# Kernel optimization log

Measured on AMD Instinct MI355X. Metric: run time of the kernel, lower is better.

## Reference

```python
import jax, jax.numpy as jnp
import numpy as np

N_NODES = 100000
N_EDGES = 1600000
N_FEAT = 128
HIDDEN = 64
N_CLASSES = 40


def setup_inputs() -> dict:
    key = jax.random.key(0)
    ks = jax.random.split(key, 4)
    x = jax.random.normal(ks[0], (N_NODES, N_FEAT), dtype=jnp.float32)
    edge_index = jax.random.randint(ks[1], (2, N_EDGES), 0, N_NODES, dtype=jnp.int64)
    # Glorot-style init like PyG GCNConv
    W1 = jax.random.normal(ks[2], (N_FEAT, HIDDEN), dtype=jnp.float32) * (1.0 / np.sqrt(N_FEAT))
    b1 = jnp.zeros((HIDDEN,), dtype=jnp.float32)
    W2 = jax.random.normal(ks[3], (HIDDEN, N_CLASSES), dtype=jnp.float32) * (1.0 / np.sqrt(HIDDEN))
    b2 = jnp.zeros((N_CLASSES,), dtype=jnp.float32)
    return {"x": x, "edge_index": edge_index, "W1": W1, "b1": b1, "W2": W2, "b2": b2}


def _gcn_conv(x, src, dst, norm, W, b, n_nodes):
    # PyG GCNConv: transform first, then normalized scatter-add aggregation
    h = x @ W                                   # [N, out]
    msg = h[src] * norm[:, None]                # [E+N, out] gather
    out = jax.ops.segment_sum(msg, dst, num_segments=n_nodes)  # scatter-add
    return out + b


def _norm_and_loops(edge_index, n_nodes):
    # add self-loops, symmetric normalization deg^{-1/2} A_hat deg^{-1/2}
    loop = jnp.arange(n_nodes, dtype=edge_index.dtype)
    src = jnp.concatenate([edge_index[0], loop])
    dst = jnp.concatenate([edge_index[1], loop])
    deg = jax.ops.segment_sum(jnp.ones_like(dst, dtype=jnp.float32), dst, num_segments=n_nodes)
    dinv = jnp.where(deg > 0, jax.lax.rsqrt(jnp.maximum(deg, 1.0)), 0.0)
    norm = dinv[src] * dinv[dst]
    return src, dst, norm


def reference(x, edge_index, W1, b1, W2, b2):
    n_nodes = x.shape[0]
    src, dst, norm = _norm_and_loops(edge_index, n_nodes)
    h = _gcn_conv(x, src, dst, norm, W1, b1, n_nodes)
    h = jax.nn.relu(h)
    h = _gcn_conv(h, src, dst, norm, W2, b2, n_nodes)
    return jax.nn.log_softmax(h, axis=1)
```

## Files before the change

### kernel.cpp

```cpp
#include <hip/hip_runtime.h>
#include <hip/hip_bf16.h>
#include <string.h>

#define N_FEAT 128
#define HIDDEN 64
#define N_CLS  40
#define SCAN_B 256
#define FILL_BLOCKS 1024
#define CHUNK_EDGES 2048

typedef __bf16 bf16x8 __attribute__((ext_vector_type(8)));
typedef float  f32x4  __attribute__((ext_vector_type(4)));

union Frag { unsigned u[4]; bf16x8 v; };

static __device__ inline int get_xcc() {
    return (int)(__builtin_amdgcn_s_getreg((3 << 11) | 20) & 7u);
}


static __device__ inline unsigned pack_bf16(float a, float b) {
    unsigned ba = __float_as_uint(a);
    unsigned bb = __float_as_uint(b);
    unsigned ra = (ba + 0x7fffu + ((ba >> 16) & 1u)) >> 16;
    unsigned rb = (bb + 0x7fffu + ((bb >> 16) & 1u)) >> 16;
    return (ra & 0xffffu) | (rb << 16);
}

static __device__ inline float2 unpack_bf16(unsigned v) {
    return make_float2(__uint_as_float(v << 16), __uint_as_float(v & 0xffff0000u));
}


__global__ void detect_layout_kernel(const int* __restrict__ ei, int* __restrict__ flag) {
    int lane = threadIdx.x;
    int v = ei[2 * lane + 1];
    unsigned long long b = __ballot(v != 0);
    if (lane == 0) flag[0] = (b == 0ull) ? 1 : 0;
}


__global__ __launch_bounds__(256) void count_kernel(const int* __restrict__ ei,
                                                    const int* __restrict__ flag,
                                                    unsigned* __restrict__ deg,
                                                    unsigned* __restrict__ ctr, int E, int N) {
    int r = get_xcc();
    int rng = (((N + 7) >> 3) + 15) & ~15;
    int lo = r * rng;
    int hi = min(N, lo + rng);
    bool is64 = (flag[0] != 0);
    const int* dstp = is64 ? (ei + 2 * E) : (ei + E);
    int stride = is64 ? 2 : 1;
    __shared__ unsigned chunk_s;
    for (;;) {
        if (threadIdx.x == 0)
            chunk_s = __hip_atomic_fetch_add(&ctr[r * 64], 1u, __ATOMIC_RELAXED,
                                             __HIP_MEMORY_SCOPE_WORKGROUP);
        __syncthreads();
        long long base = (long long)chunk_s * CHUNK_EDGES;
        __syncthreads();
        if (base >= E) break;
        int end = (int)min((long long)E, base + CHUNK_EDGES);
        for (int e = (int)base + threadIdx.x; e < end; e += 256) {
            int d = dstp[(size_t)e * stride];
            if (d >= lo && d < hi)
                __hip_atomic_fetch_add(&deg[d], 1u, __ATOMIC_RELAXED,
                                       __HIP_MEMORY_SCOPE_WORKGROUP);
        }
    }
}


__global__ void scan1_kernel(const unsigned* __restrict__ deg, unsigned* __restrict__ rowptr,
                             unsigned* __restrict__ blockSums, float* __restrict__ dinv, int N) {
    __shared__ unsigned tmp[SCAN_B];
    int i = blockIdx.x * SCAN_B + threadIdx.x;
    unsigned v = (i < N) ? deg[i] : 0u;
    if (i < N) dinv[i] = rsqrtf((float)(v + 1u));
    tmp[threadIdx.x] = v;
    __syncthreads();
#pragma unroll
    for (int off = 1; off < SCAN_B; off <<= 1) {
        unsigned t = (threadIdx.x >= off) ? tmp[threadIdx.x - off] : 0u;
        __syncthreads();
        tmp[threadIdx.x] += t;
        __syncthreads();
    }
    if (i < N) rowptr[i] = tmp[threadIdx.x] - v;
    if (threadIdx.x == SCAN_B - 1) blockSums[blockIdx.x] = tmp[threadIdx.x];
}

__global__ void scan2_kernel(unsigned* __restrict__ blockSums, int nb) {
    __shared__ unsigned tmp[512];
    unsigned v = (threadIdx.x < (unsigned)nb) ? blockSums[threadIdx.x] : 0u;
    tmp[threadIdx.x] = v;
    __syncthreads();
#pragma unroll
    for (int off = 1; off < 512; off <<= 1) {
        unsigned t = (threadIdx.x >= (unsigned)off) ? tmp[threadIdx.x - off] : 0u;
        __syncthreads();
        tmp[threadIdx.x] += t;
        __syncthreads();
    }
    if (threadIdx.x < (unsigned)nb) blockSums[threadIdx.x] = tmp[threadIdx.x] - v;
}

__global__ void scan3_kernel(unsigned* __restrict__ rowptr, const unsigned* __restrict__ blockSums,
                             unsigned* __restrict__ cursor, int N) {
    int i = blockIdx.x * SCAN_B + threadIdx.x;
    if (i < N) {
        unsigned v = rowptr[i] + blockSums[blockIdx.x];
        rowptr[i] = v;
        cursor[i] = v;
    }
}


__global__ __launch_bounds__(256) void csr_fill_kernel(const int* __restrict__ ei,
                                                       const int* __restrict__ flag,
                                                       unsigned* __restrict__ cursor,
                                                       unsigned* __restrict__ ctr,
                                                       int* __restrict__ csr_src, int E, int N) {
    int r = get_xcc();
    int rng = (((N + 7) >> 3) + 15) & ~15;
    int lo = r * rng;
    int hi = min(N, lo + rng);
    bool is64 = (flag[0] != 0);
    const int* dstp = is64 ? (ei + 2 * E) : (ei + E);
    int stride = is64 ? 2 : 1;
    __shared__ unsigned chunk_s;
    for (;;) {
        if (threadIdx.x == 0)
            chunk_s = __hip_atomic_fetch_add(&ctr[r * 64], 1u, __ATOMIC_RELAXED,
                                             __HIP_MEMORY_SCOPE_WORKGROUP);
        __syncthreads();
        long long base = (long long)chunk_s * CHUNK_EDGES;
        __syncthreads();
        if (base >= E) break;
        int end = (int)min((long long)E, base + CHUNK_EDGES);
        for (int e = (int)base + threadIdx.x; e < end; e += 256) {
            int d = dstp[(size_t)e * stride];
            if (d >= lo && d < hi) {
                int s = ei[(size_t)e * stride];
                unsigned slot = __hip_atomic_fetch_add(&cursor[d], 1u, __ATOMIC_RELAXED,
                                                       __HIP_MEMORY_SCOPE_WORKGROUP);
                csr_src[slot] = s;
            }
        }
    }
}


__global__ __launch_bounds__(256) void gemm1_mfma_kernel(const float* __restrict__ x,
                                                         const float* __restrict__ W1,
                                                         unsigned* __restrict__ h1b, int N) {
    int lane = threadIdx.x & 63;
    int quad = lane >> 4;
    int col  = lane & 15;

    Frag B[4][4];
#pragma unroll
    for (int c = 0; c < 4; ++c)
#pragma unroll
        for (int ks = 0; ks < 4; ++ks) {
            int n = c * 16 + col;
#pragma unroll
            for (int jj = 0; jj < 4; ++jj) {
                int k = ks * 32 + quad * 8 + 2 * jj;
                B[c][ks].u[jj] = pack_bf16(W1[k * HIDDEN + n], W1[(k + 1) * HIDDEN + n]);
            }
        }

    int wave_id = blockIdx.x * 4 + (threadIdx.x >> 6);
    int nwaves  = gridDim.x * 4;
    int ntiles  = (N + 15) >> 4;

    for (int rt = wave_id; rt < ntiles; rt += nwaves) {
        int rowA = rt * 16 + col;
        Frag A[4];
#pragma unroll
        for (int ks = 0; ks < 4; ++ks) {
            float4 a0 = make_float4(0.f, 0.f, 0.f, 0.f), a1 = a0;
            if (rowA < N) {
                const float4* ap = (const float4*)(x + (size_t)rowA * N_FEAT + ks * 32 + quad * 8);
                a0 = ap[0];
                a1 = ap[1];
            }
            A[ks].u[0] = pack_bf16(a0.x, a0.y);
            A[ks].u[1] = pack_bf16(a0.z, a0.w);
            A[ks].u[2] = pack_bf16(a1.x, a1.y);
            A[ks].u[3] = pack_bf16(a1.z, a1.w);
        }
        f32x4 acc[4] = {{0.f, 0.f, 0.f, 0.f}, {0.f, 0.f, 0.f, 0.f},
                        {0.f, 0.f, 0.f, 0.f}, {0.f, 0.f, 0.f, 0.f}};
#pragma unroll
        for (int ks = 0; ks < 4; ++ks)
#pragma unroll
            for (int c = 0; c < 4; ++c)
                acc[c] = __builtin_amdgcn_mfma_f32_16x16x32_bf16(A[ks].v, B[c][ks].v, acc[c], 0, 0, 0);

        int rowD = rt * 16 + quad * 4;
#pragma unroll
        for (int c = 0; c < 4; ++c)
#pragma unroll
            for (int r = 0; r < 4; ++r) {
                float v = acc[c][r];
                float nxt = __shfl_down(v, 1);
                int row = rowD + r;
                if (((lane & 1) == 0) && row < N)
                    h1b[(size_t)row * 32 + ((c * 16 + col) >> 1)] = pack_bf16(v, nxt);
            }
    }
}


__global__ __launch_bounds__(256) void gemm2_mfma_kernel(const unsigned* __restrict__ actb,
                                                         const float* __restrict__ W2,
                                                         unsigned* __restrict__ h2b, int N) {
    int lane = threadIdx.x & 63;
    int quad = lane >> 4;
    int col  = lane & 15;

    Frag B[3][2];
#pragma unroll
    for (int c = 0; c < 3; ++c)
#pragma unroll
        for (int ks = 0; ks < 2; ++ks) {
            int n = c * 16 + col;
#pragma unroll
            for (int jj = 0; jj < 4; ++jj) {
                int k = ks * 32 + quad * 8 + 2 * jj;
                float w0 = (n < N_CLS) ? W2[k * N_CLS + n] : 0.f;
                float w1 = (n < N_CLS) ? W2[(k + 1) * N_CLS + n] : 0.f;
                B[c][ks].u[jj] = pack_bf16(w0, w1);
            }
        }

    int wave_id = blockIdx.x * 4 + (threadIdx.x >> 6);
    int nwaves  = gridDim.x * 4;
    int ntiles  = (N + 15) >> 4;

    for (int rt = wave_id; rt < ntiles; rt += nwaves) {
        int rowA = rt * 16 + col;
        Frag A[2];
#pragma unroll
        for (int ks = 0; ks < 2; ++ks) {
            uint4 u = make_uint4(0u, 0u, 0u, 0u);
            if (rowA < N)
                u = *(const uint4*)(actb + (size_t)rowA * 32 + ks * 16 + quad * 4);
            A[ks].u[0] = u.x; A[ks].u[1] = u.y; A[ks].u[2] = u.z; A[ks].u[3] = u.w;
        }
        f32x4 acc[3] = {{0.f, 0.f, 0.f, 0.f}, {0.f, 0.f, 0.f, 0.f}, {0.f, 0.f, 0.f, 0.f}};
#pragma unroll
        for (int ks = 0; ks < 2; ++ks)
#pragma unroll
            for (int c = 0; c < 3; ++c)
                acc[c] = __builtin_amdgcn_mfma_f32_16x16x32_bf16(A[ks].v, B[c][ks].v, acc[c], 0, 0, 0);

        int rowD = rt * 16 + quad * 4;
#pragma unroll
        for (int c = 0; c < 3; ++c)
#pragma unroll
            for (int r = 0; r < 4; ++r) {
                float v = acc[c][r];
                float nxt = __shfl_down(v, 1);
                int row = rowD + r;
                int pair = (c * 16 + col) >> 1;
                if (((lane & 1) == 0) && pair < 20 && row < N)
                    h2b[(size_t)row * 20 + pair] = pack_bf16(v, nxt);
            }
    }
}


__global__ __launch_bounds__(256) void agg1_kernel(const unsigned* __restrict__ h1b,
                                                   const int* __restrict__ csr_src,
                                                   const unsigned* __restrict__ rowptr,
                                                   const unsigned* __restrict__ deg,
                                                   const float* __restrict__ dinv,
                                                   const float* __restrict__ b1,
                                                   unsigned* __restrict__ actb, int N) {
    int wave = threadIdx.x >> 6, lane = threadIdx.x & 63;
    int sub = lane >> 5, j = lane & 31;
    int d = blockIdx.x * 4 + wave;
    if (d >= N) return;
    float dv = dinv[d];
    float acc0 = 0.f, acc1 = 0.f;
    if (sub == 0) {
        float2 v = unpack_bf16(h1b[(size_t)d * 32 + j]);
        acc0 = dv * v.x; acc1 = dv * v.y;
    }
    unsigned beg = rowptr[d];
    int len = (int)deg[d];
    int i = 0;
    for (; i + 8 <= len; i += 8) {
        int s0 = csr_src[beg + i + sub];
        int s1 = csr_src[beg + i + 2 + sub];
        int s2 = csr_src[beg + i + 4 + sub];
        int s3 = csr_src[beg + i + 6 + sub];
        float w0 = dinv[s0], w1 = dinv[s1], w2 = dinv[s2], w3 = dinv[s3];
        unsigned v0 = h1b[(size_t)s0 * 32 + j];
        unsigned v1 = h1b[(size_t)s1 * 32 + j];
        unsigned v2 = h1b[(size_t)s2 * 32 + j];
        unsigned v3 = h1b[(size_t)s3 * 32 + j];
        float2 a0 = unpack_bf16(v0), a1 = unpack_bf16(v1);
        float2 a2 = unpack_bf16(v2), a3 = unpack_bf16(v3);
        acc0 += w0 * a0.x + w1 * a1.x + w2 * a2.x + w3 * a3.x;
        acc1 += w0 * a0.y + w1 * a1.y + w2 * a2.y + w3 * a3.y;
    }
    for (; i + 4 <= len; i += 4) {
        int sA = csr_src[beg + i + sub];
        int sB = csr_src[beg + i + 2 + sub];
        float wA = dinv[sA], wB = dinv[sB];
        float2 a = unpack_bf16(h1b[(size_t)sA * 32 + j]);
        float2 b = unpack_bf16(h1b[(size_t)sB * 32 + j]);
        acc0 += wA * a.x + wB * b.x;
        acc1 += wA * a.y + wB * b.y;
    }
    for (; i < len; i += 2) {
        int e = i + sub;
        if (e < len) {
            int s = csr_src[beg + e];
            float w = dinv[s];
            float2 a = unpack_bf16(h1b[(size_t)s * 32 + j]);
            acc0 += w * a.x;
            acc1 += w * a.y;
        }
    }
    acc0 += __shfl_xor(acc0, 32);
    acc1 += __shfl_xor(acc1, 32);
    if (sub == 0) {
        float2 bb = ((const float2*)b1)[j];
        float r0 = fmaxf(acc0 * dv + bb.x, 0.f);
        float r1 = fmaxf(acc1 * dv + bb.y, 0.f);
        actb[(size_t)d * 32 + j] = pack_bf16(r0, r1);
    }
}


__global__ __launch_bounds__(256) void agg2_lsm_kernel(const unsigned* __restrict__ h2b,
                                                       const int* __restrict__ csr_src,
                                                       const unsigned* __restrict__ rowptr,
                                                       const unsigned* __restrict__ deg,
                                                       const float* __restrict__ dinv,
                                                       const float* __restrict__ b2,
                                                       float* __restrict__ out, int N) {
    int wave = threadIdx.x >> 6, lane = threadIdx.x & 63;
    int sub = lane >> 5, j = lane & 31;
    bool act = (j < 20);
    int d = blockIdx.x * 4 + wave;
    if (d >= N) return;
    float dv = dinv[d];
    float acc0 = 0.f, acc1 = 0.f;
    if (sub == 0 && act) {
        float2 v = unpack_bf16(h2b[(size_t)d * 20 + j]);
        acc0 = dv * v.x; acc1 = dv * v.y;
    }
    unsigned beg = rowptr[d];
    int len = (int)deg[d];
    int i = 0;
    for (; i + 8 <= len; i += 8) {
        int s0 = csr_src[beg + i + sub];
        int s1 = csr_src[beg + i + 2 + sub];
        int s2 = csr_src[beg + i + 4 + sub];
        int s3 = csr_src[beg + i + 6 + sub];
        float w0 = dinv[s0], w1 = dinv[s1], w2 = dinv[s2], w3 = dinv[s3];
        if (act) {
            float2 a0 = unpack_bf16(h2b[(size_t)s0 * 20 + j]);
            float2 a1 = unpack_bf16(h2b[(size_t)s1 * 20 + j]);
            float2 a2 = unpack_bf16(h2b[(size_t)s2 * 20 + j]);
            float2 a3 = unpack_bf16(h2b[(size_t)s3 * 20 + j]);
            acc0 += w0 * a0.x + w1 * a1.x + w2 * a2.x + w3 * a3.x;
            acc1 += w0 * a0.y + w1 * a1.y + w2 * a2.y + w3 * a3.y;
        }
    }
    for (; i + 4 <= len; i += 4) {
        int sA = csr_src[beg + i + sub];
        int sB = csr_src[beg + i + 2 + sub];
        float wA = dinv[sA], wB = dinv[sB];
        if (act) {
            float2 a = unpack_bf16(h2b[(size_t)sA * 20 + j]);
            float2 b = unpack_bf16(h2b[(size_t)sB * 20 + j]);
            acc0 += wA * a.x + wB * b.x;
            acc1 += wA * a.y + wB * b.y;
        }
    }
    for (; i < len; i += 2) {
        int e = i + sub;
        if (e < len && act) {
            int s = csr_src[beg + e];
            float w = dinv[s];
            float2 a = unpack_bf16(h2b[(size_t)s * 20 + j]);
            acc0 += w * a.x;
            acc1 += w * a.y;
        }
    }
    acc0 += __shfl_xor(acc0, 32);
    acc1 += __shfl_xor(acc1, 32);
    float v0 = -1e30f, v1 = -1e30f;
    if (act) {
        float2 bb = ((const float2*)b2)[j];
        v0 = acc0 * dv + bb.x;
        v1 = acc1 * dv + bb.y;
    }
    float m = fmaxf(v0, v1);
#pragma unroll
    for (int off = 32; off > 0; off >>= 1)
        m = fmaxf(m, __shfl_xor(m, off));
    float ex = (act && sub == 0) ? (expf(v0 - m) + expf(v1 - m)) : 0.f;
#pragma unroll
    for (int off = 32; off > 0; off >>= 1)
        ex += __shfl_xor(ex, off);
    float ls = logf(ex);
    if (act && sub == 0) {
        float2* orow = (float2*)(out + (size_t)d * N_CLS);
        orow[j] = make_float2(v0 - m - ls, v1 - m - ls);
    }
}


static inline size_t align_up(size_t x) { return (x + 255) & ~(size_t)255; }

extern "C" void kernel_launch(void* const* d_in, const int* in_sizes, int n_in,
                              void* d_out, int out_size, void* d_ws, size_t ws_size,
                              hipStream_t stream) {
    const float* x  = (const float*)d_in[0];
    const int*   ei = (const int*)d_in[1];
    const float* W1 = (const float*)d_in[2];
    const float* b1 = (const float*)d_in[3];
    const float* W2 = (const float*)d_in[4];
    const float* b2 = (const float*)d_in[5];

    int N = in_sizes[0] / N_FEAT;
    int E = in_sizes[1] / 2;
    int nb = (N + SCAN_B - 1) / SCAN_B;

    char* ws = (char*)d_ws;
    int*      flag    = (int*)ws;       ws += 256;
    unsigned* ctrs    = (unsigned*)ws;  ws += 4096;
    unsigned* deg     = (unsigned*)ws;  ws += align_up((size_t)N * 4);
    float*    dinv    = (float*)ws;     ws += align_up((size_t)N * 4);
    unsigned* rowptr  = (unsigned*)ws;  ws += align_up((size_t)N * 4);
    unsigned* cursor  = (unsigned*)ws;  ws += align_up((size_t)N * 4);
    unsigned* bsums   = (unsigned*)ws;  ws += align_up((size_t)nb * 4);
    int*      csr_src = (int*)ws;       ws += align_up((size_t)E * 4);
    unsigned* h1b     = (unsigned*)ws;  ws += align_up((size_t)N * 32 * 4);
    unsigned* actb    = (unsigned*)ws;  ws += align_up((size_t)N * 32 * 4);
    unsigned* h2b     = (unsigned*)ws;  ws += align_up((size_t)N * 20 * 4);

    hipMemsetAsync(ctrs, 0, 4096, stream);
    hipMemsetAsync(deg, 0, (size_t)N * 4, stream);

    detect_layout_kernel<<<1, 64, 0, stream>>>(ei, flag);
    count_kernel<<<FILL_BLOCKS, 256, 0, stream>>>(ei, flag, deg, ctrs, E, N);

    scan1_kernel<<<nb, SCAN_B, 0, stream>>>(deg, rowptr, bsums, dinv, N);
    scan2_kernel<<<1, 512, 0, stream>>>(bsums, nb);
    scan3_kernel<<<nb, SCAN_B, 0, stream>>>(rowptr, bsums, cursor, N);
    csr_fill_kernel<<<FILL_BLOCKS, 256, 0, stream>>>(ei, flag, cursor, ctrs + 512, csr_src, E, N);

    gemm1_mfma_kernel<<<512, 256, 0, stream>>>(x, W1, h1b, N);
    agg1_kernel<<<(N + 3) / 4, 256, 0, stream>>>(h1b, csr_src, rowptr, deg, dinv, b1, actb, N);

    gemm2_mfma_kernel<<<512, 256, 0, stream>>>(actb, W2, h2b, N);
    agg2_lsm_kernel<<<(N + 3) / 4, 256, 0, stream>>>(h2b, csr_src, rowptr, deg, dinv, b2, (float*)d_out, N);
}
```

Baseline: 385.7 us.

## Build CSR via two-level bucket sort instead of per-node atomics

Replaces the per-node degree count, three-pass scan and atomic CSR fill with a coarse bucket sort over groups of 64 destinations. A shared-memory histogram counts edges per bucket, a single-block scan computes bucket offsets, edges are scattered packed (src plus local dst) into per-bucket slots, and a per-bucket kernel computes degrees, rowptr, dinv and the final local ordering in LDS. This cuts global atomic contention and launch count, but adds a temporary buffer and assumes node ids fit in 17 bits.

```diff
diff --git a/kernel.cpp b/kernel.cpp
--- a/kernel.cpp
+++ b/kernel.cpp
@@ -5,9 +5,10 @@
 #define N_FEAT 128
 #define HIDDEN 64
 #define N_CLS  40
-#define SCAN_B 256
 #define FILL_BLOCKS 1024
-#define CHUNK_EDGES 2048
+#define CHUNK_EDGES 1024
+#define B_BITS 6
+#define SRC_BITS 17
 
 typedef __bf16 bf16x8 __attribute__((ext_vector_type(8)));
 typedef float  f32x4  __attribute__((ext_vector_type(4)));
@@ -40,14 +41,67 @@
 }
 
 
-__global__ __launch_bounds__(256) void count_kernel(const int* __restrict__ ei,
-                                                    const int* __restrict__ flag,
-                                                    unsigned* __restrict__ deg,
-                                                    unsigned* __restrict__ ctr, int E, int N) {
+__global__ __launch_bounds__(256) void bucket_hist_kernel(const int* __restrict__ ei,
+                                                          const int* __restrict__ flag,
+                                                          unsigned* __restrict__ bcnt,
+                                                          int E, int nbuk) {
+    __shared__ unsigned h[2048];
+    for (int i = threadIdx.x; i < nbuk; i += 256) h[i] = 0u;
+    __syncthreads();
+    bool is64 = (flag[0] != 0);
+    const int* dstp = is64 ? (ei + 2 * E) : (ei + E);
+    int stride = is64 ? 2 : 1;
+    for (int e = blockIdx.x * 256 + threadIdx.x; e < E; e += gridDim.x * 256) {
+        int d = dstp[(size_t)e * stride];
+        atomicAdd(&h[d >> B_BITS], 1u);
+    }
+    __syncthreads();
+    for (int i = threadIdx.x; i < nbuk; i += 256)
+        if (h[i]) atomicAdd(&bcnt[i], h[i]);
+}
+
+
+__global__ __launch_bounds__(512) void bucket_scan_kernel(const unsigned* __restrict__ bcnt,
+                                                          unsigned* __restrict__ bbase,
+                                                          unsigned* __restrict__ bcur, int nbuk) {
+    __shared__ unsigned tmp[512];
+    __shared__ unsigned carry;
+    if (threadIdx.x == 0) carry = 0u;
+    __syncthreads();
+    for (int base = 0; base < nbuk; base += 512) {
+        int i = base + threadIdx.x;
+        unsigned v = (i < nbuk) ? bcnt[i] : 0u;
+        tmp[threadIdx.x] = v;
+        __syncthreads();
+#pragma unroll
+        for (int off = 1; off < 512; off <<= 1) {
+            unsigned t = (threadIdx.x >= (unsigned)off) ? tmp[threadIdx.x - off] : 0u;
+            __syncthreads();
+            tmp[threadIdx.x] += t;
+            __syncthreads();
+        }
+        unsigned excl = tmp[threadIdx.x] - v + carry;
+        if (i < nbuk) {
+            bbase[i] = excl;
+            bcur[(size_t)i * 16] = excl;
+        }
+        __syncthreads();
+        if (threadIdx.x == 511) carry += tmp[511];
+        __syncthreads();
+    }
+}
+
+
+__global__ __launch_bounds__(256) void fill_buckets_kernel(const int* __restrict__ ei,
+                                                           const int* __restrict__ flag,
+                                                           unsigned* __restrict__ bcur,
+                                                           unsigned* __restrict__ ctr,
+                                                           unsigned* __restrict__ tmpbuf,
+                                                           int E, int nbuk) {
     int r = get_xcc();
-    int rng = (((N + 7) >> 3) + 15) & ~15;
-    int lo = r * rng;
-    int hi = min(N, lo + rng);
+    int bpx = (nbuk + 7) >> 3;
+    int blo = r * bpx;
+    int bhi = min(nbuk, blo + bpx);
     bool is64 = (flag[0] != 0);
     const int* dstp = is64 ? (ei + 2 * E) : (ei + E);
     int stride = is64 ? 2 : 1;
@@ -63,90 +117,59 @@
         int end = (int)min((long long)E, base + CHUNK_EDGES);
         for (int e = (int)base + threadIdx.x; e < end; e += 256) {
             int d = dstp[(size_t)e * stride];
-            if (d >= lo && d < hi)
-                __hip_atomic_fetch_add(&deg[d], 1u, __ATOMIC_RELAXED,
-                                       __HIP_MEMORY_SCOPE_WORKGROUP);
-        }
-    }
-}
-
-
-__global__ void scan1_kernel(const unsigned* __restrict__ deg, unsigned* __restrict__ rowptr,
-                             unsigned* __restrict__ blockSums, float* __restrict__ dinv, int N) {
-    __shared__ unsigned tmp[SCAN_B];
-    int i = blockIdx.x * SCAN_B + threadIdx.x;
-    unsigned v = (i < N) ? deg[i] : 0u;
-    if (i < N) dinv[i] = rsqrtf((float)(v + 1u));
-    tmp[threadIdx.x] = v;
-    __syncthreads();
-#pragma unroll
-    for (int off = 1; off < SCAN_B; off <<= 1) {
-        unsigned t = (threadIdx.x >= off) ? tmp[threadIdx.x - off] : 0u;
-        __syncthreads();
-        tmp[threadIdx.x] += t;
-        __syncthreads();
-    }
-    if (i < N) rowptr[i] = tmp[threadIdx.x] - v;
-    if (threadIdx.x == SCAN_B - 1) blockSums[blockIdx.x] = tmp[threadIdx.x];
-}
-
-__global__ void scan2_kernel(unsigned* __restrict__ blockSums, int nb) {
-    __shared__ unsigned tmp[512];
-    unsigned v = (threadIdx.x < (unsigned)nb) ? blockSums[threadIdx.x] : 0u;
-    tmp[threadIdx.x] = v;
-    __syncthreads();
-#pragma unroll
-    for (int off = 1; off < 512; off <<= 1) {
-        unsigned t = (threadIdx.x >= (unsigned)off) ? tmp[threadIdx.x - off] : 0u;
-        __syncthreads();
-        tmp[threadIdx.x] += t;
-        __syncthreads();
-    }
-    if (threadIdx.x < (unsigned)nb) blockSums[threadIdx.x] = tmp[threadIdx.x] - v;
-}
-
-__global__ void scan3_kernel(unsigned* __restrict__ rowptr, const unsigned* __restrict__ blockSums,
-                             unsigned* __restrict__ cursor, int N) {
-    int i = blockIdx.x * SCAN_B + threadIdx.x;
-    if (i < N) {
-        unsigned v = rowptr[i] + blockSums[blockIdx.x];
-        rowptr[i] = v;
-        cursor[i] = v;
-    }
-}
-
-
-__global__ __launch_bounds__(256) void csr_fill_kernel(const int* __restrict__ ei,
-                                                       const int* __restrict__ flag,
-                                                       unsigned* __restrict__ cursor,
-                                                       unsigned* __restrict__ ctr,
-                                                       int* __restrict__ csr_src, int E, int N) {
-    int r = get_xcc();
-    int rng = (((N + 7) >> 3) + 15) & ~15;
-    int lo = r * rng;
-    int hi = min(N, lo + rng);
-    bool is64 = (flag[0] != 0);
-    const int* dstp = is64 ? (ei + 2 * E) : (ei + E);
-    int stride = is64 ? 2 : 1;
-    __shared__ unsigned chunk_s;
-    for (;;) {
-        if (threadIdx.x == 0)
-            chunk_s = __hip_atomic_fetch_add(&ctr[r * 64], 1u, __ATOMIC_RELAXED,
-                                             __HIP_MEMORY_SCOPE_WORKGROUP);
-        __syncthreads();
-        long long base = (long long)chunk_s * CHUNK_EDGES;
-        __syncthreads();
-        if (base >= E) break;
-        int end = (int)min((long long)E, base + CHUNK_EDGES);
-        for (int e = (int)base + threadIdx.x; e < end; e += 256) {
-            int d = dstp[(size_t)e * stride];
-            if (d >= lo && d < hi) {
+            int b = d >> B_BITS;
+            if (b >= blo && b < bhi) {
                 int s = ei[(size_t)e * stride];
-                unsigned slot = __hip_atomic_fetch_add(&cursor[d], 1u, __ATOMIC_RELAXED,
+                unsigned val = (unsigned)s | ((unsigned)(d & ((1 << B_BITS) - 1)) << SRC_BITS);
+                unsigned slot = __hip_atomic_fetch_add(&bcur[(size_t)b * 16], 1u, __ATOMIC_RELAXED,
                                                        __HIP_MEMORY_SCOPE_WORKGROUP);
-                csr_src[slot] = s;
-            }
-        }
+                tmpbuf[slot] = val;
+            }
+        }
+    }
+}
+
+
+__global__ __launch_bounds__(256) void bucket_to_csr_kernel(const unsigned* __restrict__ tmpbuf,
+                                                            const unsigned* __restrict__ bbase,
+                                                            unsigned* __restrict__ deg,
+                                                            unsigned* __restrict__ rowptr,
+                                                            float* __restrict__ dinv,
+                                                            int* __restrict__ csr_src,
+                                                            int nbuk, int N, int E) {
+    int b = blockIdx.x;
+    int tid = threadIdx.x;
+    unsigned beg = bbase[b];
+    unsigned end = (b + 1 < nbuk) ? bbase[b + 1] : (unsigned)E;
+    int d0 = b << B_BITS;
+    const int ND = 1 << B_BITS;
+    __shared__ unsigned hist[ND], scn[ND], cur[ND];
+    if (tid < ND) { hist[tid] = 0u; cur[tid] = 0u; }
+    __syncthreads();
+    for (unsigned i = beg + tid; i < end; i += 256)
+        atomicAdd(&hist[tmpbuf[i] >> SRC_BITS], 1u);
+    __syncthreads();
+    if (tid == 0) {
+        unsigned run = 0;
+        for (int k = 0; k < ND; ++k) { scn[k] = run; run += hist[k]; }
+    }
+    __syncthreads();
+    if (tid < ND) {
+        int d = d0 + tid;
+        if (d < N) {
+            unsigned dg = hist[tid];
+            deg[d] = dg;
+            dinv[d] = rsqrtf((float)(dg + 1u));
+            rowptr[d] = beg + scn[tid];
+        }
+    }
+    __syncthreads();
+    for (unsigned i = beg + tid; i < end; i += 256) {
+        unsigned v = tmpbuf[i];
+        unsigned dl = v >> SRC_BITS;
+        unsigned s = v & ((1u << SRC_BITS) - 1u);
+        unsigned p = atomicAdd(&cur[dl], 1u);
+        csr_src[beg + scn[dl] + p] = (int)s;
     }
 }
 
@@ -433,31 +456,31 @@
 
     int N = in_sizes[0] / N_FEAT;
     int E = in_sizes[1] / 2;
-    int nb = (N + SCAN_B - 1) / SCAN_B;
+    int nbuk = (N + (1 << B_BITS) - 1) >> B_BITS;
 
     char* ws = (char*)d_ws;
     int*      flag    = (int*)ws;       ws += 256;
     unsigned* ctrs    = (unsigned*)ws;  ws += 4096;
+    unsigned* bcnt    = (unsigned*)ws;  ws += align_up((size_t)nbuk * 4);
+    unsigned* bbase   = (unsigned*)ws;  ws += align_up((size_t)nbuk * 4);
+    unsigned* bcur    = (unsigned*)ws;  ws += align_up((size_t)nbuk * 64);
     unsigned* deg     = (unsigned*)ws;  ws += align_up((size_t)N * 4);
     float*    dinv    = (float*)ws;     ws += align_up((size_t)N * 4);
     unsigned* rowptr  = (unsigned*)ws;  ws += align_up((size_t)N * 4);
-    unsigned* cursor  = (unsigned*)ws;  ws += align_up((size_t)N * 4);
-    unsigned* bsums   = (unsigned*)ws;  ws += align_up((size_t)nb * 4);
+    unsigned* tmpbuf  = (unsigned*)ws;  ws += align_up((size_t)E * 4);
     int*      csr_src = (int*)ws;       ws += align_up((size_t)E * 4);
     unsigned* h1b     = (unsigned*)ws;  ws += align_up((size_t)N * 32 * 4);
     unsigned* actb    = (unsigned*)ws;  ws += align_up((size_t)N * 32 * 4);
     unsigned* h2b     = (unsigned*)ws;  ws += align_up((size_t)N * 20 * 4);
 
     hipMemsetAsync(ctrs, 0, 4096, stream);
-    hipMemsetAsync(deg, 0, (size_t)N * 4, stream);
+    hipMemsetAsync(bcnt, 0, (size_t)nbuk * 4, stream);
 
     detect_layout_kernel<<<1, 64, 0, stream>>>(ei, flag);
-    count_kernel<<<FILL_BLOCKS, 256, 0, stream>>>(ei, flag, deg, ctrs, E, N);
-
-    scan1_kernel<<<nb, SCAN_B, 0, stream>>>(deg, rowptr, bsums, dinv, N);
-    scan2_kernel<<<1, 512, 0, stream>>>(bsums, nb);
-    scan3_kernel<<<nb, SCAN_B, 0, stream>>>(rowptr, bsums, cursor, N);
-    csr_fill_kernel<<<FILL_BLOCKS, 256, 0, stream>>>(ei, flag, cursor, ctrs + 512, csr_src, E, N);
+    bucket_hist_kernel<<<256, 256, 0, stream>>>(ei, flag, bcnt, E, nbuk);
+    bucket_scan_kernel<<<1, 512, 0, stream>>>(bcnt, bbase, bcur, nbuk);
+    fill_buckets_kernel<<<FILL_BLOCKS, 256, 0, stream>>>(ei, flag, bcur, ctrs, tmpbuf, E, nbuk);
+    bucket_to_csr_kernel<<<nbuk, 256, 0, stream>>>(tmpbuf, bbase, deg, rowptr, dinv, csr_src, nbuk, N, E);
 
     gemm1_mfma_kernel<<<512, 256, 0, stream>>>(x, W1, h1b, N);
     agg1_kernel<<<(N + 3) / 4, 256, 0, stream>>>(h1b, csr_src, rowptr, deg, dinv, b1, actb, N);
```

Measured after the change: 352.6 us. -8.6%, faster.

## Pre-partition edges by destination XCC range into per-XCC buckets

Applied to the files above, without the earlier changes.

Adds a split kernel that reads the edge list once and stages (src,dst) pairs in shared memory, then flushes them into eight per-XCC buckets selected by destination range. The degree-count and CSR-placement kernels then each read only their own bucket instead of every XCC scanning all edges and discarding most of them. This is meant to cut the redundant full edge-list reads done once per XCC in both passes. In exchange it adds an extra kernel pass, a bucket buffer of about 8 bytes per edge, and shared-memory staging with block-wide syncs.

```diff
diff --git a/kernel.cpp b/kernel.cpp
--- a/kernel.cpp
+++ b/kernel.cpp
@@ -6,8 +6,11 @@
 #define HIDDEN 64
 #define N_CLS  40
 #define SCAN_B 256
-#define FILL_BLOCKS 1024
-#define CHUNK_EDGES 2048
+#define SPLIT_BLOCKS 640
+#define SPLIT_CAP 512
+#define SPLIT_FLUSH 256
+#define PROC_BLOCKS 1024
+#define CHUNK_ENT 2048
 
 typedef __bf16 bf16x8 __attribute__((ext_vector_type(8)));
 typedef float  f32x4  __attribute__((ext_vector_type(4)));
@@ -40,32 +43,88 @@
 }
 
 
-__global__ __launch_bounds__(256) void count_kernel(const int* __restrict__ ei,
+__global__ __launch_bounds__(256) void split_kernel(const int* __restrict__ ei,
                                                     const int* __restrict__ flag,
-                                                    unsigned* __restrict__ deg,
-                                                    unsigned* __restrict__ ctr, int E, int N) {
-    int r = get_xcc();
-    int rng = (((N + 7) >> 3) + 15) & ~15;
-    int lo = r * rng;
-    int hi = min(N, lo + rng);
+                                                    unsigned* __restrict__ gcur,
+                                                    uint2* __restrict__ mb,
+                                                    int E, int rng, int cap) {
+    __shared__ uint2 stage[8][SPLIT_CAP];
+    __shared__ unsigned cnt[8];
+    __shared__ unsigned fbase;
+    if (threadIdx.x < 8) cnt[threadIdx.x] = 0u;
+    __syncthreads();
+
     bool is64 = (flag[0] != 0);
     const int* dstp = is64 ? (ei + 2 * E) : (ei + E);
     int stride = is64 ? 2 : 1;
+
+    int per = (E + SPLIT_BLOCKS - 1) / SPLIT_BLOCKS;
+    int base = blockIdx.x * per;
+    int end  = min(E, base + per);
+
+    for (int it = base; it < end; it += 256) {
+        int e = it + threadIdx.x;
+        if (e < end) {
+            int d = dstp[(size_t)e * stride];
+            int s = ei[(size_t)e * stride];
+            unsigned r = (unsigned)d / (unsigned)rng;
+            unsigned idx = atomicAdd(&cnt[r], 1u);
+            stage[r][idx] = make_uint2((unsigned)s, (unsigned)d);
+        }
+        __syncthreads();
+        for (int r = 0; r < 8; ++r) {
+            if (cnt[r] >= SPLIT_FLUSH) {
+                if (threadIdx.x == 0)
+                    fbase = atomicAdd(&gcur[r * 16], (unsigned)SPLIT_FLUSH);
+                __syncthreads();
+                mb[(size_t)r * cap + fbase + threadIdx.x] = stage[r][threadIdx.x];
+                unsigned tail = cnt[r] - SPLIT_FLUSH;
+                uint2 tv;
+                if (threadIdx.x < tail) tv = stage[r][SPLIT_FLUSH + threadIdx.x];
+                __syncthreads();
+                if (threadIdx.x < tail) stage[r][threadIdx.x] = tv;
+                if (threadIdx.x == 0) cnt[r] = tail;
+                __syncthreads();
+            }
+        }
+    }
+    for (int r = 0; r < 8; ++r) {
+        unsigned c = cnt[r];
+        if (c > 0) {
+            if (threadIdx.x == 0)
+                fbase = atomicAdd(&gcur[r * 16], c);
+            __syncthreads();
+            for (unsigned off = 0; off < c; off += 256)
+                if (threadIdx.x < c - off)
+                    mb[(size_t)r * cap + fbase + off + threadIdx.x] = stage[r][off + threadIdx.x];
+        }
+        __syncthreads();
+    }
+}
+
+
+__global__ __launch_bounds__(256) void count2_kernel(const uint2* __restrict__ mb,
+                                                     const unsigned* __restrict__ gcur,
+                                                     unsigned* __restrict__ ctr,
+                                                     unsigned* __restrict__ deg,
+                                                     int cap) {
+    int r = get_xcc();
+    unsigned size = gcur[r * 16];
+    const uint2* my = mb + (size_t)r * cap;
     __shared__ unsigned chunk_s;
     for (;;) {
         if (threadIdx.x == 0)
-            chunk_s = __hip_atomic_fetch_add(&ctr[r * 64], 1u, __ATOMIC_RELAXED,
+            chunk_s = __hip_atomic_fetch_add(&ctr[r * 16], 1u, __ATOMIC_RELAXED,
                                              __HIP_MEMORY_SCOPE_WORKGROUP);
         __syncthreads();
-        long long base = (long long)chunk_s * CHUNK_EDGES;
-        __syncthreads();
-        if (base >= E) break;
-        int end = (int)min((long long)E, base + CHUNK_EDGES);
-        for (int e = (int)base + threadIdx.x; e < end; e += 256) {
-            int d = dstp[(size_t)e * stride];
-            if (d >= lo && d < hi)
-                __hip_atomic_fetch_add(&deg[d], 1u, __ATOMIC_RELAXED,
-                                       __HIP_MEMORY_SCOPE_WORKGROUP);
+        unsigned base = chunk_s * CHUNK_ENT;
+        __syncthreads();
+        if (base >= size) break;
+        unsigned end = min(size, base + CHUNK_ENT);
+        for (unsigned i = base + threadIdx.x; i < end; i += 256) {
+            unsigned d = my[i].y;
+            __hip_atomic_fetch_add(&deg[d], 1u, __ATOMIC_RELAXED,
+                                   __HIP_MEMORY_SCOPE_WORKGROUP);
         }
     }
 }
@@ -116,36 +175,30 @@
 }
 
 
-__global__ __launch_bounds__(256) void csr_fill_kernel(const int* __restrict__ ei,
-                                                       const int* __restrict__ flag,
-                                                       unsigned* __restrict__ cursor,
-                                                       unsigned* __restrict__ ctr,
-                                                       int* __restrict__ csr_src, int E, int N) {
+__global__ __launch_bounds__(256) void place_kernel(const uint2* __restrict__ mb,
+                                                    const unsigned* __restrict__ gcur,
+                                                    unsigned* __restrict__ ctr,
+                                                    unsigned* __restrict__ cursor,
+                                                    int* __restrict__ csr_src,
+                                                    int cap) {
     int r = get_xcc();
-    int rng = (((N + 7) >> 3) + 15) & ~15;
-    int lo = r * rng;
-    int hi = min(N, lo + rng);
-    bool is64 = (flag[0] != 0);
-    const int* dstp = is64 ? (ei + 2 * E) : (ei + E);
-    int stride = is64 ? 2 : 1;
+    unsigned size = gcur[r * 16];
+    const uint2* my = mb + (size_t)r * cap;
     __shared__ unsigned chunk_s;
     for (;;) {
         if (threadIdx.x == 0)
-            chunk_s = __hip_atomic_fetch_add(&ctr[r * 64], 1u, __ATOMIC_RELAXED,
+            chunk_s = __hip_atomic_fetch_add(&ctr[r * 16], 1u, __ATOMIC_RELAXED,
                                              __HIP_MEMORY_SCOPE_WORKGROUP);
         __syncthreads();
-        long long base = (long long)chunk_s * CHUNK_EDGES;
-        __syncthreads();
-        if (base >= E) break;
-        int end = (int)min((long long)E, base + CHUNK_EDGES);
-        for (int e = (int)base + threadIdx.x; e < end; e += 256) {
-            int d = dstp[(size_t)e * stride];
-            if (d >= lo && d < hi) {
-                int s = ei[(size_t)e * stride];
-                unsigned slot = __hip_atomic_fetch_add(&cursor[d], 1u, __ATOMIC_RELAXED,
-                                                       __HIP_MEMORY_SCOPE_WORKGROUP);
-                csr_src[slot] = s;
-            }
+        unsigned base = chunk_s * CHUNK_ENT;
+        __syncthreads();
+        if (base >= size) break;
+        unsigned end = min(size, base + CHUNK_ENT);
+        for (unsigned i = base + threadIdx.x; i < end; i += 256) {
+            uint2 v = my[i];
+            unsigned slot = __hip_atomic_fetch_add(&cursor[v.y], 1u, __ATOMIC_RELAXED,
+                                                   __HIP_MEMORY_SCOPE_WORKGROUP);
+            csr_src[slot] = (int)v.x;
         }
     }
 }
@@ -434,30 +487,39 @@
     int N = in_sizes[0] / N_FEAT;
     int E = in_sizes[1] / 2;
     int nb = (N + SCAN_B - 1) / SCAN_B;
+    int rng = (((N + 7) >> 3) + 15) & ~15;
+    int cap = E / 8 + 65536;
 
     char* ws = (char*)d_ws;
     int*      flag    = (int*)ws;       ws += 256;
-    unsigned* ctrs    = (unsigned*)ws;  ws += 4096;
+    unsigned* ctrs    = (unsigned*)ws;  ws += 2048;
     unsigned* deg     = (unsigned*)ws;  ws += align_up((size_t)N * 4);
     float*    dinv    = (float*)ws;     ws += align_up((size_t)N * 4);
     unsigned* rowptr  = (unsigned*)ws;  ws += align_up((size_t)N * 4);
     unsigned* cursor  = (unsigned*)ws;  ws += align_up((size_t)N * 4);
     unsigned* bsums   = (unsigned*)ws;  ws += align_up((size_t)nb * 4);
+    uint2*    mb      = (uint2*)ws;     ws += align_up((size_t)8 * cap * 8);
     int*      csr_src = (int*)ws;       ws += align_up((size_t)E * 4);
     unsigned* h1b     = (unsigned*)ws;  ws += align_up((size_t)N * 32 * 4);
     unsigned* actb    = (unsigned*)ws;  ws += align_up((size_t)N * 32 * 4);
     unsigned* h2b     = (unsigned*)ws;  ws += align_up((size_t)N * 20 * 4);
 
-    hipMemsetAsync(ctrs, 0, 4096, stream);
+    unsigned* gcur = ctrs;
+    unsigned* ctrA = ctrs + 128;
+    unsigned* ctrB = ctrs + 256;
+
+    hipMemsetAsync(ctrs, 0, 2048, stream);
     hipMemsetAsync(deg, 0, (size_t)N * 4, stream);
 
     detect_layout_kernel<<<1, 64, 0, stream>>>(ei, flag);
-    count_kernel<<<FILL_BLOCKS, 256, 0, stream>>>(ei, flag, deg, ctrs, E, N);
+    split_kernel<<<SPLIT_BLOCKS, 256, 0, stream>>>(ei, flag, gcur, mb, E, rng, cap);
+    count2_kernel<<<PROC_BLOCKS, 256, 0, stream>>>(mb, gcur, ctrA, deg, cap);
 
     scan1_kernel<<<nb, SCAN_B, 0, stream>>>(deg, rowptr, bsums, dinv, N);
     scan2_kernel<<<1, 512, 0, stream>>>(bsums, nb);
     scan3_kernel<<<nb, SCAN_B, 0, stream>>>(rowptr, bsums, cursor, N);
-    csr_fill_kernel<<<FILL_BLOCKS, 256, 0, stream>>>(ei, flag, cursor, ctrs + 512, csr_src, E, N);
+
+    place_kernel<<<PROC_BLOCKS, 256, 0, stream>>>(mb, gcur, ctrB, cursor, csr_src, cap);
 
     gemm1_mfma_kernel<<<512, 256, 0, stream>>>(x, W1, h1b, N);
     agg1_kernel<<<(N + 3) / 4, 256, 0, stream>>>(h1b, csr_src, rowptr, deg, dinv, b1, actb, N);
```

New measurement: 421.0 us. 9.2% more time.
